# Kernel optimization log

Hardware: AMD Instinct MI355X
Metric: run time of the kernel (lower is better)

## Reference

```python
import jax, jax.numpy as jnp
import numpy as np

N_NODES = 1_000_000
N_UPD = 200_000
D_MEM = 172
D_MSG = 172


def setup_inputs() -> dict:
    key = jax.random.key(0)
    ks = jax.random.split(key, 8)
    memory = jax.random.normal(ks[0], (N_NODES, D_MEM), dtype=jnp.float32)
    last_update = jnp.zeros((N_NODES,), dtype=jnp.float32)
    # unique node ids (no duplicates, as guaranteed by the caller in the original code)
    unique_node_ids = jax.random.permutation(ks[1], N_NODES)[:N_UPD].astype(jnp.int64)
    unique_messages = jax.random.normal(ks[2], (N_UPD, D_MSG), dtype=jnp.float32)
    timestamps = jax.random.uniform(ks[3], (N_UPD,), dtype=jnp.float32) * 1e6
    s_ih = 1.0 / np.sqrt(D_MEM)
    weight_ih = jax.random.uniform(ks[4], (3 * D_MEM, D_MSG), jnp.float32, -s_ih, s_ih)
    weight_hh = jax.random.uniform(ks[5], (3 * D_MEM, D_MEM), jnp.float32, -s_ih, s_ih)
    bias_ih = jax.random.uniform(ks[6], (3 * D_MEM,), jnp.float32, -s_ih, s_ih)
    bias_hh = jax.random.uniform(ks[7], (3 * D_MEM,), jnp.float32, -s_ih, s_ih)
    return {
        "memory": memory,
        "last_update": last_update,
        "unique_node_ids": unique_node_ids,
        "unique_messages": unique_messages,
        "timestamps": timestamps,
        "weight_ih": weight_ih,
        "weight_hh": weight_hh,
        "bias_ih": bias_ih,
        "bias_hh": bias_hh,
    }


def _gru_cell(x, h, weight_ih, weight_hh, bias_ih, bias_hh):
    # PyTorch GRUCell, gate order: reset, update, new
    gi = x @ weight_ih.T + bias_ih          # [M, 3H]
    gh = h @ weight_hh.T + bias_hh          # [M, 3H]
    i_r, i_z, i_n = jnp.split(gi, 3, axis=-1)
    h_r, h_z, h_n = jnp.split(gh, 3, axis=-1)
    r = jax.nn.sigmoid(i_r + h_r)
    z = jax.nn.sigmoid(i_z + h_z)
    n = jnp.tanh(i_n + r * h_n)
    return n + z * (h - n)                  # (1-z)*n + z*h


def reference(memory, last_update, unique_node_ids, unique_messages, timestamps,
              weight_ih, weight_hh, bias_ih, bias_hh):
    # gather rows of the node memory for the updated nodes
    h = memory[unique_node_ids]                                   # [M, D]
    h_new = _gru_cell(unique_messages, h, weight_ih, weight_hh, bias_ih, bias_hh)
    # scatter updated rows back (ids are unique)
    updated_memory = memory.at[unique_node_ids].set(h_new)        # [N, D]
    updated_last_update = last_update.at[unique_node_ids].set(timestamps)
    # original module returns memory with the singleton middle dim restored
    return updated_memory[:, None, :], updated_last_update
```

## Files before the change

### kernel.cpp

```cpp
#include <hip/hip_runtime.h>

typedef __attribute__((ext_vector_type(8))) short short8;
typedef __attribute__((ext_vector_type(4))) float f32x4;

#define N_NODES 1000000
#define N_UPD   200000
#define D       172
#define BM      64
#define LDA     360
#define KSTEPS  11
#define NTILES  48
#define KSLICE  (NTILES*512)
#define GRU_BLOCKS (N_UPD / BM)
#define NM4 43000000
#define BPACK_USHORTS (KSTEPS*KSLICE)
#define BIAS_OFF  (BPACK_USHORTS*2)
#define MASK_OFF  (BIAS_OFF + 688*4)
#define WS_NEED   (MASK_OFF + N_NODES)

__device__ __forceinline__ unsigned short f2bf(float f) {
  union { float f; unsigned u; } v; v.f = f;
  unsigned r = v.u + 0x7FFFu + ((v.u >> 16) & 1u);
  return (unsigned short)(r >> 16);
}
__device__ __forceinline__ float bf2f(unsigned short h) {
  union { unsigned u; float f; } v; v.u = ((unsigned)h) << 16;
  return v.f;
}
__device__ __forceinline__ ushort4 f2bf4(float4 v) {
  return make_ushort4(f2bf(v.x), f2bf(v.y), f2bf(v.z), f2bf(v.w));
}

__global__ void prep_kernel(const float* __restrict__ wih, const float* __restrict__ whh,
                            const float* __restrict__ bih, const float* __restrict__ bhh,
                            unsigned short* __restrict__ Bpack, float* __restrict__ bias4,
                            uint4* __restrict__ mask16) {
  int gid = blockIdx.x * 256 + threadIdx.x;
  if (gid < 688) {
    int which = gid / 172, j = gid % 172;
    float v;
    if (which == 0)      v = bih[j]       + bhh[j];
    else if (which == 1) v = bih[172 + j] + bhh[172 + j];
    else if (which == 2) v = bih[344 + j];
    else                 v = bhh[344 + j];
    bias4[gid] = v;
  }
  if (gid < N_NODES / 16) mask16[gid] = make_uint4(0, 0, 0, 0);
  if (gid >= BPACK_USHORTS) return;
  int e  = gid & 7;
  int l  = (gid >> 3) & 63;
  int nt = (gid >> 9) % NTILES;
  int ks = gid / KSLICE;
  int k  = ks * 32 + ((l >> 4) << 3) + e;
  int c  = l & 15;
  int w  = nt / 12, tl = nt % 12;
  int gate = tl / 3, ti = tl % 3;
  int j = w * 48 + ti * 16 + c;
  float v = 0.f;
  if (j < D) {
    if (gate == 0) {
      if (k < D)        v = wih[j * D + k];
      else if (k < 2*D) v = whh[j * D + (k - D)];
    } else if (gate == 1) {
      if (k < D)        v = wih[(D + j) * D + k];
      else if (k < 2*D) v = whh[(D + j) * D + (k - D)];
    } else if (gate == 2) {
      if (k < D)        v = wih[(2*D + j) * D + k];
    } else {
      if (k >= D && k < 2*D) v = whh[(2*D + j) * D + (k - D)];
    }
  }
  Bpack[gid] = f2bf(v);
}

__global__ void mask_set_kernel(const int* __restrict__ ids, unsigned char* __restrict__ mask) {
  int i = blockIdx.x * 256 + threadIdx.x;
  if (i < N_UPD) mask[ids[i]] = 1;
}

__global__ void copy_kernel(const float4* __restrict__ mem4, const float4* __restrict__ lu4,
                            float4* __restrict__ out4, float4* __restrict__ outlu4) {
  const long NL4 = N_NODES / 4;
  long stride = (long)gridDim.x * blockDim.x;
  for (long i = (long)blockIdx.x * blockDim.x + threadIdx.x; i < NM4 + NL4; i += stride) {
    if (i < NM4) out4[i] = mem4[i];
    else         outlu4[i - NM4] = lu4[i - NM4];
  }
}

__global__ __launch_bounds__(256)
void copy_masked_kernel(const float4* __restrict__ mem4, const float* __restrict__ lu,
                        const unsigned char* __restrict__ mask,
                        float4* __restrict__ out4, float* __restrict__ outlu) {
  const unsigned stride = gridDim.x * 256;
  for (unsigned i = blockIdx.x * 256 + threadIdx.x; i < NM4; i += stride) {
    unsigned row = i / 43u;
    if (!mask[row]) out4[i] = mem4[i];
  }
  for (unsigned j = blockIdx.x * 256 + threadIdx.x; j < N_NODES; j += stride) {
    if (!mask[j]) outlu[j] = lu[j];
  }
}

__global__ __launch_bounds__(512, 4)
void gru64_kernel(const float* __restrict__ memory, const float* __restrict__ msgs,
                  const int* __restrict__ ids, const float* __restrict__ ts,
                  const unsigned short* __restrict__ Bpack, const float* __restrict__ bias4,
                  float* __restrict__ out_mem, float* __restrict__ out_lu) {
  __shared__ unsigned short At[BM * LDA];
  const int tid  = threadIdx.x;
  const int m0   = blockIdx.x * BM;
  const int wave = tid >> 6, lane = tid & 63;
  const int g = lane >> 4, c = lane & 15;
  const int wm = wave >> 2, wc = wave & 3;

  const float4* x4 = (const float4*)msgs + (size_t)m0 * 43;
  float4 xv[6], hv[6];
  #pragma unroll
  for (int i = 0; i < 6; ++i) {
    int s = tid + i * 512;
    if (i < 5 || s < 2752) xv[i] = x4[s];
  }
  #pragma unroll
  for (int i = 0; i < 6; ++i) {
    int s = tid + i * 512;
    if (i < 5 || s < 2752) {
      int row = s / 43, seg = s - row * 43;
      hv[i] = ((const float4*)(memory + (size_t)ids[m0 + row] * D))[seg];
    }
  }
  #pragma unroll
  for (int i = 0; i < 6; ++i) {
    int s = tid + i * 512;
    if (i < 5 || s < 2752) {
      int row = s / 43, seg = s - row * 43;
      *(ushort4*)&At[row * LDA + seg * 4]       = f2bf4(xv[i]);
      *(ushort4*)&At[row * LDA + 172 + seg * 4] = f2bf4(hv[i]);
    }
  }
  if (tid < BM) {
    *(uint4*)&At[tid * LDA + 344] = make_uint4(0, 0, 0, 0);
    out_lu[ids[m0 + tid]] = ts[m0 + tid];
  }
  __syncthreads();

  const int ar0 = (wm * 32 + c) * LDA;
  const int ar1 = ar0 + 16 * LDA;
  const short8* Bp = (const short8*)Bpack;

  #pragma unroll 1
  for (int ti = 0; ti < 3; ++ti) {
    if (wc == 3 && ti == 2) continue;
    const short8* bp = Bp + (size_t)((wc * 12 + ti) * 64 + lane);

    f32x4 Cr0={0,0,0,0}, Cr1={0,0,0,0};
    f32x4 Cz0={0,0,0,0}, Cz1={0,0,0,0};
    f32x4 Ci0={0,0,0,0}, Ci1={0,0,0,0};
    f32x4 Ch0={0,0,0,0}, Ch1={0,0,0,0};

    #pragma unroll 2
    for (int ks = 0; ks < KSTEPS; ++ks) {
      const short8* bk = bp + ks * 3072;
      short8 br = bk[0];
      short8 bz = bk[192];
      short8 bi = bk[384];
      short8 bh = bk[576];
      short8 a0 = *(const short8*)&At[ar0 + ks * 32 + g * 8];
      short8 a1 = *(const short8*)&At[ar1 + ks * 32 + g * 8];
      Cr0 = __builtin_amdgcn_mfma_f32_16x16x32_bf16(a0, br, Cr0, 0, 0, 0);
      Cr1 = __builtin_amdgcn_mfma_f32_16x16x32_bf16(a1, br, Cr1, 0, 0, 0);
      Cz0 = __builtin_amdgcn_mfma_f32_16x16x32_bf16(a0, bz, Cz0, 0, 0, 0);
      Cz1 = __builtin_amdgcn_mfma_f32_16x16x32_bf16(a1, bz, Cz1, 0, 0, 0);
      Ci0 = __builtin_amdgcn_mfma_f32_16x16x32_bf16(a0, bi, Ci0, 0, 0, 0);
      Ci1 = __builtin_amdgcn_mfma_f32_16x16x32_bf16(a1, bi, Ci1, 0, 0, 0);
      Ch0 = __builtin_amdgcn_mfma_f32_16x16x32_bf16(a0, bh, Ch0, 0, 0, 0);
      Ch1 = __builtin_amdgcn_mfma_f32_16x16x32_bf16(a1, bh, Ch1, 0, 0, 0);
    }

    const int j = wc * 48 + ti * 16 + c;
    if (j < D) {
      const float b_r = bias4[j];
      const float b_z = bias4[172 + j];
      const float b_i = bias4[344 + j];
      const float b_h = bias4[516 + j];
      #pragma unroll
      for (int r = 0; r < 4; ++r) {
        {
          const int row_local = wm * 32 + g * 4 + r;
          float* orow = out_mem + (size_t)ids[m0 + row_local] * D;
          float ho = bf2f(At[row_local * LDA + 172 + j]);
          float rr = 1.f / (1.f + __expf(-(Cr0[r] + b_r)));
          float zz = 1.f / (1.f + __expf(-(Cz0[r] + b_z)));
          float e2 = __expf(2.f * (Ci0[r] + b_i + rr * (Ch0[r] + b_h)));
          float nn = 1.f - 2.f / (e2 + 1.f);
          orow[j] = nn + zz * (ho - nn);
        }
        {
          const int row_local = wm * 32 + 16 + g * 4 + r;
          float* orow = out_mem + (size_t)ids[m0 + row_local] * D;
          float ho = bf2f(At[row_local * LDA + 172 + j]);
          float rr = 1.f / (1.f + __expf(-(Cr1[r] + b_r)));
          float zz = 1.f / (1.f + __expf(-(Cz1[r] + b_z)));
          float e2 = __expf(2.f * (Ci1[r] + b_i + rr * (Ch1[r] + b_h)));
          float nn = 1.f - 2.f / (e2 + 1.f);
          orow[j] = nn + zz * (ho - nn);
        }
      }
    }
  }
}

extern "C" void kernel_launch(void* const* d_in, const int* in_sizes, int n_in,
                              void* d_out, int out_size, void* d_ws, size_t ws_size,
                              hipStream_t stream) {
  const float* memory      = (const float*)d_in[0];
  const float* last_update = (const float*)d_in[1];
  const int*   ids         = (const int*)  d_in[2];
  const float* msgs        = (const float*)d_in[3];
  const float* ts          = (const float*)d_in[4];
  const float* wih         = (const float*)d_in[5];
  const float* whh         = (const float*)d_in[6];
  const float* bih         = (const float*)d_in[7];
  const float* bhh         = (const float*)d_in[8];

  float* out_mem = (float*)d_out;
  float* out_lu  = out_mem + (size_t)N_NODES * D;

  unsigned short* Bpack = (unsigned short*)d_ws;
  float* bias4 = (float*)((char*)d_ws + BIAS_OFF);
  unsigned char* mask = (unsigned char*)d_ws + MASK_OFF;

  prep_kernel<<<BPACK_USHORTS / 256, 256, 0, stream>>>(wih, whh, bih, bhh, Bpack, bias4,
                                                       (uint4*)mask);
  if (ws_size >= WS_NEED) {
    mask_set_kernel<<<(N_UPD + 255) / 256, 256, 0, stream>>>(ids, mask);
    copy_masked_kernel<<<2048, 256, 0, stream>>>((const float4*)memory, last_update, mask,
                                                 (float4*)out_mem, out_lu);
  } else {
    copy_kernel<<<4096, 256, 0, stream>>>((const float4*)memory, (const float4*)last_update,
                                          (float4*)out_mem, (float4*)out_lu);
  }
  gru64_kernel<<<GRU_BLOCKS, 512, 0, stream>>>(memory, msgs, ids, ts, Bpack, bias4,
                                               out_mem, out_lu);
}
```

Baseline: 492.7 us.

## Fuse masked copy and GRU into one kernel with interleaved block roles

Merges the masked memory-copy kernel and the GRU gather/compute/scatter kernel into a single launch. Blocks are assigned roles in cycles of five groups of eight, three doing GRU tiles and two doing strided copy work. The bandwidth-bound copy can then overlap with the compute-heavy GRU, and one launch and its tail are removed. In exchange, copy blocks now use 512 threads and the GRU kernel's launch bounds and LDS allocation, which may limit how many copy blocks fit per CU.

```diff
diff --git a/kernel.cpp b/kernel.cpp
--- a/kernel.cpp
+++ b/kernel.cpp
@@ -12,6 +12,9 @@
 #define NTILES  48
 #define KSLICE  (NTILES*512)
 #define GRU_BLOCKS (N_UPD / BM)
+#define NCYC    131
+#define NCOPY_BLOCKS (NCYC*2*8)
+#define COPY_STRIDE (NCOPY_BLOCKS*512)
 #define NM4 43000000
 #define BPACK_USHORTS (KSTEPS*KSLICE)
 #define BIAS_OFF  (BPACK_USHORTS*2)
@@ -88,28 +91,38 @@
   }
 }
 
-__global__ __launch_bounds__(256)
-void copy_masked_kernel(const float4* __restrict__ mem4, const float* __restrict__ lu,
-                        const unsigned char* __restrict__ mask,
-                        float4* __restrict__ out4, float* __restrict__ outlu) {
-  const unsigned stride = gridDim.x * 256;
-  for (unsigned i = blockIdx.x * 256 + threadIdx.x; i < NM4; i += stride) {
-    unsigned row = i / 43u;
-    if (!mask[row]) out4[i] = mem4[i];
-  }
-  for (unsigned j = blockIdx.x * 256 + threadIdx.x; j < N_NODES; j += stride) {
-    if (!mask[j]) outlu[j] = lu[j];
-  }
-}
-
 __global__ __launch_bounds__(512, 4)
-void gru64_kernel(const float* __restrict__ memory, const float* __restrict__ msgs,
-                  const int* __restrict__ ids, const float* __restrict__ ts,
-                  const unsigned short* __restrict__ Bpack, const float* __restrict__ bias4,
-                  float* __restrict__ out_mem, float* __restrict__ out_lu) {
+void fused_kernel(const float* __restrict__ memory, const float* __restrict__ last_update,
+                  const float* __restrict__ msgs, const int* __restrict__ ids,
+                  const float* __restrict__ ts, const unsigned short* __restrict__ Bpack,
+                  const float* __restrict__ bias4, const unsigned char* __restrict__ mask,
+                  float* __restrict__ out_mem, float* __restrict__ out_lu, int has_copy) {
   __shared__ unsigned short At[BM * LDA];
-  const int tid  = threadIdx.x;
-  const int m0   = blockIdx.x * BM;
+  const int tid = threadIdx.x;
+  int idx;
+  if (has_copy) {
+    const int g8 = blockIdx.x >> 3, b7 = blockIdx.x & 7;
+    const int cyc = g8 / 5, pos = g8 - cyc * 5;
+    if (pos >= 3) {
+      const int cblk = (cyc * 2 + (pos - 3)) * 8 + b7;
+      const float4* mem4 = (const float4*)memory;
+      float4* out4 = (float4*)out_mem;
+      for (unsigned i = (unsigned)cblk * 512 + tid; i < NM4; i += COPY_STRIDE) {
+        unsigned row = i / 43u;
+        if (!mask[row]) out4[i] = mem4[i];
+      }
+      for (unsigned j = (unsigned)cblk * 512 + tid; j < N_NODES; j += COPY_STRIDE) {
+        if (!mask[j]) out_lu[j] = last_update[j];
+      }
+      return;
+    }
+    idx = (cyc * 3 + pos) * 8 + b7;
+    if (idx >= GRU_BLOCKS) return;
+  } else {
+    idx = blockIdx.x;
+  }
+
+  const int m0   = idx * BM;
   const int wave = tid >> 6, lane = tid & 63;
   const int g = lane >> 4, c = lane & 15;
   const int wm = wave >> 2, wc = wave & 3;
@@ -234,12 +247,12 @@
                                                        (uint4*)mask);
   if (ws_size >= WS_NEED) {
     mask_set_kernel<<<(N_UPD + 255) / 256, 256, 0, stream>>>(ids, mask);
-    copy_masked_kernel<<<2048, 256, 0, stream>>>((const float4*)memory, last_update, mask,
-                                                 (float4*)out_mem, out_lu);
+    fused_kernel<<<NCYC * 5 * 8, 512, 0, stream>>>(memory, last_update, msgs, ids, ts,
+                                                   Bpack, bias4, mask, out_mem, out_lu, 1);
   } else {
     copy_kernel<<<4096, 256, 0, stream>>>((const float4*)memory, (const float4*)last_update,
                                           (float4*)out_mem, (float4*)out_lu);
-  }
-  gru64_kernel<<<GRU_BLOCKS, 512, 0, stream>>>(memory, msgs, ids, ts, Bpack, bias4,
-                                               out_mem, out_lu);
-}
+    fused_kernel<<<GRU_BLOCKS, 512, 0, stream>>>(memory, last_update, msgs, ids, ts,
+                                                 Bpack, bias4, mask, out_mem, out_lu, 0);
+  }
+}
```

After: 513.3 us. 1.04x slower.

## Halve GRU block to 4 waves, each computing all 64 rows for B reuse

Applied to the files above, without the earlier changes.

The GRU kernel now uses 256 threads (4 waves) instead of 512. Each wave covers all four 16-row M tiles for its column slice, so every weight fragment loaded from global memory feeds 4 MFMAs instead of 2, halving B-operand traffic per block. In exchange each thread holds twice as many accumulators and does more staging loads, which raises register pressure. The launch bounds change to (256,3), so occupancy and latency hiding may drop.

```diff
diff --git a/kernel.cpp b/kernel.cpp
--- a/kernel.cpp
+++ b/kernel.cpp
@@ -102,7 +102,7 @@
   }
 }
 
-__global__ __launch_bounds__(512, 4)
+__global__ __launch_bounds__(256, 3)
 void gru64_kernel(const float* __restrict__ memory, const float* __restrict__ msgs,
                   const int* __restrict__ ids, const float* __restrict__ ts,
                   const unsigned short* __restrict__ Bpack, const float* __restrict__ bias4,
@@ -110,32 +110,39 @@
   __shared__ unsigned short At[BM * LDA];
   const int tid  = threadIdx.x;
   const int m0   = blockIdx.x * BM;
-  const int wave = tid >> 6, lane = tid & 63;
+  const int wc   = tid >> 6, lane = tid & 63;
   const int g = lane >> 4, c = lane & 15;
-  const int wm = wave >> 2, wc = wave & 3;
-
-  const float4* x4 = (const float4*)msgs + (size_t)m0 * 43;
-  float4 xv[6], hv[6];
-  #pragma unroll
-  for (int i = 0; i < 6; ++i) {
-    int s = tid + i * 512;
-    if (i < 5 || s < 2752) xv[i] = x4[s];
-  }
-  #pragma unroll
-  for (int i = 0; i < 6; ++i) {
-    int s = tid + i * 512;
-    if (i < 5 || s < 2752) {
-      int row = s / 43, seg = s - row * 43;
+
+  {
+    const float4* x4 = (const float4*)msgs + (size_t)m0 * 43;
+    float4 xv[11];
+    #pragma unroll
+    for (int i = 0; i < 11; ++i) {
+      int s = tid + i * 256; int sc = s < 2752 ? s : 2751;
+      xv[i] = x4[sc];
+    }
+    #pragma unroll
+    for (int i = 0; i < 11; ++i) {
+      int s = tid + i * 256;
+      if (s < 2752) {
+        int row = s / 43, seg = s - row * 43;
+        *(ushort4*)&At[row * LDA + seg * 4] = f2bf4(xv[i]);
+      }
+    }
+    float4 hv[11];
+    #pragma unroll
+    for (int i = 0; i < 11; ++i) {
+      int s = tid + i * 256; int sc = s < 2752 ? s : 2751;
+      int row = sc / 43, seg = sc - row * 43;
       hv[i] = ((const float4*)(memory + (size_t)ids[m0 + row] * D))[seg];
     }
-  }
-  #pragma unroll
-  for (int i = 0; i < 6; ++i) {
-    int s = tid + i * 512;
-    if (i < 5 || s < 2752) {
-      int row = s / 43, seg = s - row * 43;
-      *(ushort4*)&At[row * LDA + seg * 4]       = f2bf4(xv[i]);
-      *(ushort4*)&At[row * LDA + 172 + seg * 4] = f2bf4(hv[i]);
+    #pragma unroll
+    for (int i = 0; i < 11; ++i) {
+      int s = tid + i * 256;
+      if (s < 2752) {
+        int row = s / 43, seg = s - row * 43;
+        *(ushort4*)&At[row * LDA + 172 + seg * 4] = f2bf4(hv[i]);
+      }
     }
   }
   if (tid < BM) {
@@ -144,8 +151,7 @@
   }
   __syncthreads();
 
-  const int ar0 = (wm * 32 + c) * LDA;
-  const int ar1 = ar0 + 16 * LDA;
+  const int ar = c * LDA;
   const short8* Bp = (const short8*)Bpack;
 
   #pragma unroll 1
@@ -153,10 +159,10 @@
     if (wc == 3 && ti == 2) continue;
     const short8* bp = Bp + (size_t)((wc * 12 + ti) * 64 + lane);
 
-    f32x4 Cr0={0,0,0,0}, Cr1={0,0,0,0};
-    f32x4 Cz0={0,0,0,0}, Cz1={0,0,0,0};
-    f32x4 Ci0={0,0,0,0}, Ci1={0,0,0,0};
-    f32x4 Ch0={0,0,0,0}, Ch1={0,0,0,0};
+    f32x4 Cr0={0,0,0,0}, Cr1={0,0,0,0}, Cr2={0,0,0,0}, Cr3={0,0,0,0};
+    f32x4 Cz0={0,0,0,0}, Cz1={0,0,0,0}, Cz2={0,0,0,0}, Cz3={0,0,0,0};
+    f32x4 Ci0={0,0,0,0}, Ci1={0,0,0,0}, Ci2={0,0,0,0}, Ci3={0,0,0,0};
+    f32x4 Ch0={0,0,0,0}, Ch1={0,0,0,0}, Ch2={0,0,0,0}, Ch3={0,0,0,0};
 
     #pragma unroll 2
     for (int ks = 0; ks < KSTEPS; ++ks) {
@@ -165,16 +171,27 @@
       short8 bz = bk[192];
       short8 bi = bk[384];
       short8 bh = bk[576];
-      short8 a0 = *(const short8*)&At[ar0 + ks * 32 + g * 8];
-      short8 a1 = *(const short8*)&At[ar1 + ks * 32 + g * 8];
+      const int ao = ar + ks * 32 + g * 8;
+      short8 a0 = *(const short8*)&At[ao];
+      short8 a1 = *(const short8*)&At[ao + 16 * LDA];
+      short8 a2 = *(const short8*)&At[ao + 32 * LDA];
+      short8 a3 = *(const short8*)&At[ao + 48 * LDA];
       Cr0 = __builtin_amdgcn_mfma_f32_16x16x32_bf16(a0, br, Cr0, 0, 0, 0);
       Cr1 = __builtin_amdgcn_mfma_f32_16x16x32_bf16(a1, br, Cr1, 0, 0, 0);
+      Cr2 = __builtin_amdgcn_mfma_f32_16x16x32_bf16(a2, br, Cr2, 0, 0, 0);
+      Cr3 = __builtin_amdgcn_mfma_f32_16x16x32_bf16(a3, br, Cr3, 0, 0, 0);
       Cz0 = __builtin_amdgcn_mfma_f32_16x16x32_bf16(a0, bz, Cz0, 0, 0, 0);
       Cz1 = __builtin_amdgcn_mfma_f32_16x16x32_bf16(a1, bz, Cz1, 0, 0, 0);
+      Cz2 = __builtin_amdgcn_mfma_f32_16x16x32_bf16(a2, bz, Cz2, 0, 0, 0);
+      Cz3 = __builtin_amdgcn_mfma_f32_16x16x32_bf16(a3, bz, Cz3, 0, 0, 0);
       Ci0 = __builtin_amdgcn_mfma_f32_16x16x32_bf16(a0, bi, Ci0, 0, 0, 0);
       Ci1 = __builtin_amdgcn_mfma_f32_16x16x32_bf16(a1, bi, Ci1, 0, 0, 0);
+      Ci2 = __builtin_amdgcn_mfma_f32_16x16x32_bf16(a2, bi, Ci2, 0, 0, 0);
+      Ci3 = __builtin_amdgcn_mfma_f32_16x16x32_bf16(a3, bi, Ci3, 0, 0, 0);
       Ch0 = __builtin_amdgcn_mfma_f32_16x16x32_bf16(a0, bh, Ch0, 0, 0, 0);
       Ch1 = __builtin_amdgcn_mfma_f32_16x16x32_bf16(a1, bh, Ch1, 0, 0, 0);
+      Ch2 = __builtin_amdgcn_mfma_f32_16x16x32_bf16(a2, bh, Ch2, 0, 0, 0);
+      Ch3 = __builtin_amdgcn_mfma_f32_16x16x32_bf16(a3, bh, Ch3, 0, 0, 0);
     }
 
     const int j = wc * 48 + ti * 16 + c;
@@ -183,29 +200,23 @@
       const float b_z = bias4[172 + j];
       const float b_i = bias4[344 + j];
       const float b_h = bias4[516 + j];
-      #pragma unroll
-      for (int r = 0; r < 4; ++r) {
-        {
-          const int row_local = wm * 32 + g * 4 + r;
-          float* orow = out_mem + (size_t)ids[m0 + row_local] * D;
-          float ho = bf2f(At[row_local * LDA + 172 + j]);
-          float rr = 1.f / (1.f + __expf(-(Cr0[r] + b_r)));
-          float zz = 1.f / (1.f + __expf(-(Cz0[r] + b_z)));
-          float e2 = __expf(2.f * (Ci0[r] + b_i + rr * (Ch0[r] + b_h)));
-          float nn = 1.f - 2.f / (e2 + 1.f);
-          orow[j] = nn + zz * (ho - nn);
-        }
-        {
-          const int row_local = wm * 32 + 16 + g * 4 + r;
-          float* orow = out_mem + (size_t)ids[m0 + row_local] * D;
-          float ho = bf2f(At[row_local * LDA + 172 + j]);
-          float rr = 1.f / (1.f + __expf(-(Cr1[r] + b_r)));
-          float zz = 1.f / (1.f + __expf(-(Cz1[r] + b_z)));
-          float e2 = __expf(2.f * (Ci1[r] + b_i + rr * (Ch1[r] + b_h)));
-          float nn = 1.f - 2.f / (e2 + 1.f);
-          orow[j] = nn + zz * (ho - nn);
-        }
+#define DO_MT(MT, CR, CZ, CI, CH)                                                  \
+      _Pragma("unroll")                                                            \
+      for (int r = 0; r < 4; ++r) {                                                \
+        const int row_local = (MT) * 16 + g * 4 + r;                               \
+        float* orow = out_mem + (size_t)ids[m0 + row_local] * D;                   \
+        float ho = bf2f(At[row_local * LDA + 172 + j]);                            \
+        float rr = 1.f / (1.f + __expf(-(CR[r] + b_r)));                           \
+        float zz = 1.f / (1.f + __expf(-(CZ[r] + b_z)));                           \
+        float e2 = __expf(2.f * (CI[r] + b_i + rr * (CH[r] + b_h)));               \
+        float nn = 1.f - 2.f / (e2 + 1.f);                                         \
+        orow[j] = nn + zz * (ho - nn);                                             \
       }
+      DO_MT(0, Cr0, Cz0, Ci0, Ch0)
+      DO_MT(1, Cr1, Cz1, Ci1, Ch1)
+      DO_MT(2, Cr2, Cz2, Ci2, Ch2)
+      DO_MT(3, Cr3, Cz3, Ci3, Ch3)
+#undef DO_MT
     }
   }
 }
@@ -240,6 +251,6 @@
     copy_kernel<<<4096, 256, 0, stream>>>((const float4*)memory, (const float4*)last_update,
                                           (float4*)out_mem, (float4*)out_lu);
   }
-  gru64_kernel<<<GRU_BLOCKS, 512, 0, stream>>>(memory, msgs, ids, ts, Bpack, bias4,
+  gru64_kernel<<<GRU_BLOCKS, 256, 0, stream>>>(memory, msgs, ids, ts, Bpack, bias4,
                                                out_mem, out_lu);
 }
```

New measurement: 511.1 us. 3.7% more time.

## Fuse masked copy into persistent GRU kernel to overlap copy with MFMA

Applied to the files above, without the earlier changes.

Merges the masked bulk memory copy and the GRU gather/MFMA/scatter into one persistent kernel with a fixed grid of 512 blocks. Each block loops over GRU tiles and, after each tile, copies a matching slab of non-updated memory rows and last_update entries. The aim is to remove a separate bandwidth-bound kernel launch and overlap the streaming copy with compute-bound GRU work. The cost is fewer resident blocks, since the grid shrinks from 3125 to 512, plus an extra barrier per tile, which could reduce latency hiding.

```diff
diff --git a/kernel.cpp b/kernel.cpp
--- a/kernel.cpp
+++ b/kernel.cpp
@@ -11,8 +11,11 @@
 #define KSTEPS  11
 #define NTILES  48
 #define KSLICE  (NTILES*512)
-#define GRU_BLOCKS (N_UPD / BM)
-#define NM4 43000000
+#define GRU_TILES (N_UPD / BM)
+#define GRID    512
+#define SLAB4   13760
+#define SLABLU  320
+#define NM4     43000000
 #define BPACK_USHORTS (KSTEPS*KSLICE)
 #define BIAS_OFF  (BPACK_USHORTS*2)
 #define MASK_OFF  (BIAS_OFF + 688*4)
@@ -88,125 +91,134 @@
   }
 }
 
-__global__ __launch_bounds__(256)
-void copy_masked_kernel(const float4* __restrict__ mem4, const float* __restrict__ lu,
-                        const unsigned char* __restrict__ mask,
-                        float4* __restrict__ out4, float* __restrict__ outlu) {
-  const unsigned stride = gridDim.x * 256;
-  for (unsigned i = blockIdx.x * 256 + threadIdx.x; i < NM4; i += stride) {
-    unsigned row = i / 43u;
-    if (!mask[row]) out4[i] = mem4[i];
-  }
-  for (unsigned j = blockIdx.x * 256 + threadIdx.x; j < N_NODES; j += stride) {
-    if (!mask[j]) outlu[j] = lu[j];
-  }
-}
-
+template<int HAS_COPY>
 __global__ __launch_bounds__(512, 4)
-void gru64_kernel(const float* __restrict__ memory, const float* __restrict__ msgs,
-                  const int* __restrict__ ids, const float* __restrict__ ts,
-                  const unsigned short* __restrict__ Bpack, const float* __restrict__ bias4,
+void fused_kernel(const float* __restrict__ memory, const float* __restrict__ last_update,
+                  const float* __restrict__ msgs, const int* __restrict__ ids,
+                  const float* __restrict__ ts, const unsigned short* __restrict__ Bpack,
+                  const float* __restrict__ bias4, const unsigned char* __restrict__ mask,
                   float* __restrict__ out_mem, float* __restrict__ out_lu) {
   __shared__ unsigned short At[BM * LDA];
   const int tid  = threadIdx.x;
-  const int m0   = blockIdx.x * BM;
   const int wave = tid >> 6, lane = tid & 63;
   const int g = lane >> 4, c = lane & 15;
   const int wm = wave >> 2, wc = wave & 3;
-
-  const float4* x4 = (const float4*)msgs + (size_t)m0 * 43;
-  float4 xv[6], hv[6];
-  #pragma unroll
-  for (int i = 0; i < 6; ++i) {
-    int s = tid + i * 512;
-    if (i < 5 || s < 2752) xv[i] = x4[s];
-  }
-  #pragma unroll
-  for (int i = 0; i < 6; ++i) {
-    int s = tid + i * 512;
-    if (i < 5 || s < 2752) {
-      int row = s / 43, seg = s - row * 43;
-      hv[i] = ((const float4*)(memory + (size_t)ids[m0 + row] * D))[seg];
-    }
-  }
-  #pragma unroll
-  for (int i = 0; i < 6; ++i) {
-    int s = tid + i * 512;
-    if (i < 5 || s < 2752) {
-      int row = s / 43, seg = s - row * 43;
-      *(ushort4*)&At[row * LDA + seg * 4]       = f2bf4(xv[i]);
-      *(ushort4*)&At[row * LDA + 172 + seg * 4] = f2bf4(hv[i]);
-    }
-  }
-  if (tid < BM) {
-    *(uint4*)&At[tid * LDA + 344] = make_uint4(0, 0, 0, 0);
-    out_lu[ids[m0 + tid]] = ts[m0 + tid];
-  }
-  __syncthreads();
-
   const int ar0 = (wm * 32 + c) * LDA;
   const int ar1 = ar0 + 16 * LDA;
   const short8* Bp = (const short8*)Bpack;
-
-  #pragma unroll 1
-  for (int ti = 0; ti < 3; ++ti) {
-    if (wc == 3 && ti == 2) continue;
-    const short8* bp = Bp + (size_t)((wc * 12 + ti) * 64 + lane);
-
-    f32x4 Cr0={0,0,0,0}, Cr1={0,0,0,0};
-    f32x4 Cz0={0,0,0,0}, Cz1={0,0,0,0};
-    f32x4 Ci0={0,0,0,0}, Ci1={0,0,0,0};
-    f32x4 Ch0={0,0,0,0}, Ch1={0,0,0,0};
-
-    #pragma unroll 2
-    for (int ks = 0; ks < KSTEPS; ++ks) {
-      const short8* bk = bp + ks * 3072;
-      short8 br = bk[0];
-      short8 bz = bk[192];
-      short8 bi = bk[384];
-      short8 bh = bk[576];
-      short8 a0 = *(const short8*)&At[ar0 + ks * 32 + g * 8];
-      short8 a1 = *(const short8*)&At[ar1 + ks * 32 + g * 8];
-      Cr0 = __builtin_amdgcn_mfma_f32_16x16x32_bf16(a0, br, Cr0, 0, 0, 0);
-      Cr1 = __builtin_amdgcn_mfma_f32_16x16x32_bf16(a1, br, Cr1, 0, 0, 0);
-      Cz0 = __builtin_amdgcn_mfma_f32_16x16x32_bf16(a0, bz, Cz0, 0, 0, 0);
-      Cz1 = __builtin_amdgcn_mfma_f32_16x16x32_bf16(a1, bz, Cz1, 0, 0, 0);
-      Ci0 = __builtin_amdgcn_mfma_f32_16x16x32_bf16(a0, bi, Ci0, 0, 0, 0);
-      Ci1 = __builtin_amdgcn_mfma_f32_16x16x32_bf16(a1, bi, Ci1, 0, 0, 0);
-      Ch0 = __builtin_amdgcn_mfma_f32_16x16x32_bf16(a0, bh, Ch0, 0, 0, 0);
-      Ch1 = __builtin_amdgcn_mfma_f32_16x16x32_bf16(a1, bh, Ch1, 0, 0, 0);
-    }
-
-    const int j = wc * 48 + ti * 16 + c;
-    if (j < D) {
-      const float b_r = bias4[j];
-      const float b_z = bias4[172 + j];
-      const float b_i = bias4[344 + j];
-      const float b_h = bias4[516 + j];
+  const float4* mem4 = (const float4*)memory;
+  float4* out4 = (float4*)out_mem;
+
+  for (int s = blockIdx.x; s < GRU_TILES; s += GRID) {
+    const int m0 = s * BM;
+
+    {
+      const float4* x4 = (const float4*)msgs + (size_t)m0 * 43;
+      float4 xv[6], hv[6];
       #pragma unroll
-      for (int r = 0; r < 4; ++r) {
-        {
-          const int row_local = wm * 32 + g * 4 + r;
-          float* orow = out_mem + (size_t)ids[m0 + row_local] * D;
-          float ho = bf2f(At[row_local * LDA + 172 + j]);
-          float rr = 1.f / (1.f + __expf(-(Cr0[r] + b_r)));
-          float zz = 1.f / (1.f + __expf(-(Cz0[r] + b_z)));
-          float e2 = __expf(2.f * (Ci0[r] + b_i + rr * (Ch0[r] + b_h)));
-          float nn = 1.f - 2.f / (e2 + 1.f);
-          orow[j] = nn + zz * (ho - nn);
+      for (int i = 0; i < 6; ++i) {
+        int q = tid + i * 512;
+        if (i < 5 || q < 2752) xv[i] = x4[q];
+      }
+      #pragma unroll
+      for (int i = 0; i < 6; ++i) {
+        int q = tid + i * 512;
+        if (i < 5 || q < 2752) {
+          int row = q / 43, seg = q - row * 43;
+          hv[i] = ((const float4*)(memory + (size_t)ids[m0 + row] * D))[seg];
         }
-        {
-          const int row_local = wm * 32 + 16 + g * 4 + r;
-          float* orow = out_mem + (size_t)ids[m0 + row_local] * D;
-          float ho = bf2f(At[row_local * LDA + 172 + j]);
-          float rr = 1.f / (1.f + __expf(-(Cr1[r] + b_r)));
-          float zz = 1.f / (1.f + __expf(-(Cz1[r] + b_z)));
-          float e2 = __expf(2.f * (Ci1[r] + b_i + rr * (Ch1[r] + b_h)));
-          float nn = 1.f - 2.f / (e2 + 1.f);
-          orow[j] = nn + zz * (ho - nn);
+      }
+      #pragma unroll
+      for (int i = 0; i < 6; ++i) {
+        int q = tid + i * 512;
+        if (i < 5 || q < 2752) {
+          int row = q / 43, seg = q - row * 43;
+          *(ushort4*)&At[row * LDA + seg * 4]       = f2bf4(xv[i]);
+          *(ushort4*)&At[row * LDA + 172 + seg * 4] = f2bf4(hv[i]);
         }
       }
-    }
+      if (tid < BM) {
+        *(uint4*)&At[tid * LDA + 344] = make_uint4(0, 0, 0, 0);
+        out_lu[ids[m0 + tid]] = ts[m0 + tid];
+      }
+    }
+    __syncthreads();
+
+    #pragma unroll 1
+    for (int ti = 0; ti < 3; ++ti) {
+      if (wc == 3 && ti == 2) continue;
+      const short8* bp = Bp + (size_t)((wc * 12 + ti) * 64 + lane);
+
+      f32x4 Cr0={0,0,0,0}, Cr1={0,0,0,0};
+      f32x4 Cz0={0,0,0,0}, Cz1={0,0,0,0};
+      f32x4 Ci0={0,0,0,0}, Ci1={0,0,0,0};
+      f32x4 Ch0={0,0,0,0}, Ch1={0,0,0,0};
+
+      #pragma unroll 2
+      for (int ks = 0; ks < KSTEPS; ++ks) {
+        short8 a0 = *(const short8*)&At[ar0 + ks * 32 + g * 8];
+        short8 a1 = *(const short8*)&At[ar1 + ks * 32 + g * 8];
+        const short8* bk = bp + ks * 3072;
+        short8 br = bk[0];
+        short8 bz = bk[192];
+        short8 bi = bk[384];
+        short8 bh = bk[576];
+        Cr0 = __builtin_amdgcn_mfma_f32_16x16x32_bf16(a0, br, Cr0, 0, 0, 0);
+        Cr1 = __builtin_amdgcn_mfma_f32_16x16x32_bf16(a1, br, Cr1, 0, 0, 0);
+        Cz0 = __builtin_amdgcn_mfma_f32_16x16x32_bf16(a0, bz, Cz0, 0, 0, 0);
+        Cz1 = __builtin_amdgcn_mfma_f32_16x16x32_bf16(a1, bz, Cz1, 0, 0, 0);
+        Ci0 = __builtin_amdgcn_mfma_f32_16x16x32_bf16(a0, bi, Ci0, 0, 0, 0);
+        Ci1 = __builtin_amdgcn_mfma_f32_16x16x32_bf16(a1, bi, Ci1, 0, 0, 0);
+        Ch0 = __builtin_amdgcn_mfma_f32_16x16x32_bf16(a0, bh, Ch0, 0, 0, 0);
+        Ch1 = __builtin_amdgcn_mfma_f32_16x16x32_bf16(a1, bh, Ch1, 0, 0, 0);
+      }
+
+      const int j = wc * 48 + ti * 16 + c;
+      if (j < D) {
+        const float b_r = bias4[j];
+        const float b_z = bias4[172 + j];
+        const float b_i = bias4[344 + j];
+        const float b_h = bias4[516 + j];
+        #pragma unroll
+        for (int r = 0; r < 4; ++r) {
+          {
+            const int row_local = wm * 32 + g * 4 + r;
+            float* orow = out_mem + (size_t)ids[m0 + row_local] * D;
+            float ho = bf2f(At[row_local * LDA + 172 + j]);
+            float rr = 1.f / (1.f + __expf(-(Cr0[r] + b_r)));
+            float zz = 1.f / (1.f + __expf(-(Cz0[r] + b_z)));
+            float e2 = __expf(2.f * (Ci0[r] + b_i + rr * (Ch0[r] + b_h)));
+            float nn = 1.f - 2.f / (e2 + 1.f);
+            orow[j] = nn + zz * (ho - nn);
+          }
+          {
+            const int row_local = wm * 32 + 16 + g * 4 + r;
+            float* orow = out_mem + (size_t)ids[m0 + row_local] * D;
+            float ho = bf2f(At[row_local * LDA + 172 + j]);
+            float rr = 1.f / (1.f + __expf(-(Cr1[r] + b_r)));
+            float zz = 1.f / (1.f + __expf(-(Cz1[r] + b_z)));
+            float e2 = __expf(2.f * (Ci1[r] + b_i + rr * (Ch1[r] + b_h)));
+            float nn = 1.f - 2.f / (e2 + 1.f);
+            orow[j] = nn + zz * (ho - nn);
+          }
+        }
+      }
+    }
+
+    if (HAS_COPY) {
+      const unsigned base = (unsigned)s * SLAB4;
+      #pragma unroll 1
+      for (int i = tid; i < SLAB4; i += 512) {
+        unsigned idx = base + i;
+        unsigned row = idx / 43u;
+        if (!mask[row]) out4[idx] = mem4[idx];
+      }
+      if (tid < SLABLU) {
+        unsigned jj = (unsigned)s * SLABLU + tid;
+        if (!mask[jj]) out_lu[jj] = last_update[jj];
+      }
+    }
+    __syncthreads();
   }
 }
 
@@ -234,12 +246,12 @@
                                                        (uint4*)mask);
   if (ws_size >= WS_NEED) {
     mask_set_kernel<<<(N_UPD + 255) / 256, 256, 0, stream>>>(ids, mask);
-    copy_masked_kernel<<<2048, 256, 0, stream>>>((const float4*)memory, last_update, mask,
-                                                 (float4*)out_mem, out_lu);
+    fused_kernel<1><<<GRID, 512, 0, stream>>>(memory, last_update, msgs, ids, ts,
+                                              Bpack, bias4, mask, out_mem, out_lu);
   } else {
     copy_kernel<<<4096, 256, 0, stream>>>((const float4*)memory, (const float4*)last_update,
                                           (float4*)out_mem, (float4*)out_lu);
-  }
-  gru64_kernel<<<GRU_BLOCKS, 512, 0, stream>>>(memory, msgs, ids, ts, Bpack, bias4,
-                                               out_mem, out_lu);
-}
+    fused_kernel<0><<<GRID, 512, 0, stream>>>(memory, last_update, msgs, ids, ts,
+                                              Bpack, bias4, mask, out_mem, out_lu);
+  }
+}
```

Result: slower. 584.0 us (+18.5%).
